# Optimization experiments

Hardware: AMD Instinct MI355X
Metric: run time of the kernel (lower is better)

Reference implementation:

```python
import jax, jax.numpy as jnp
import numpy as np

N_NODES = 50000
N_EDGES = 800000
D_IN = 128
D_OUT = 128
NUM_RELS = 100


def setup_inputs() -> dict:
    key = jax.random.key(0)
    k1, k2, k3, k4, k5, k6, k7 = jax.random.split(key, 7)
    h = jax.random.normal(k1, (N_NODES, D_IN), dtype=jnp.float32)
    W = jax.random.normal(k2, (D_IN, D_OUT), dtype=jnp.float32) * 0.05
    attn = jax.random.normal(k3, (2 * D_OUT,), dtype=jnp.float32) * 0.05
    rel_emb = jax.random.normal(k4, (NUM_RELS, 1), dtype=jnp.float32)
    src = jax.random.randint(k5, (N_EDGES,), 0, N_NODES, dtype=jnp.int32)
    dst = jax.random.randint(k6, (N_EDGES,), 0, N_NODES, dtype=jnp.int32)
    etype = jax.random.randint(k7, (N_EDGES,), 0, NUM_RELS, dtype=jnp.int32)
    return {"h": h, "W": W, "attn": attn, "rel_emb": rel_emb,
            "src": src, "dst": dst, "etype": etype}


def reference(h, W, attn, rel_emb, src, dst, etype):
    # h: [N, d_in], W: [d_in, d_out], attn: [2*d_out], rel_emb: [R, 1]
    # src/dst/etype: [E]
    N = h.shape[0]
    d = W.shape[1]
    # padding_idx=0 in nn.Embedding -> row 0 is zero
    rel_table = rel_emb.at[0].set(0.0)
    z = h @ W  # [N, d_out]
    # attn_fc([z_src, z_dst]) = z_src @ a_l + z_dst @ a_r (split the concat-linear)
    s_src = z @ attn[:d]  # [N]
    s_dst = z @ attn[d:]  # [N]
    e = jax.nn.leaky_relu(s_src[src] + s_dst[dst])  # [E], slope 0.01 as in torch
    # segment softmax over incoming edges of each dst node
    m = jax.ops.segment_max(e, dst, num_segments=N)  # [N]
    ex = jnp.exp(e - m[dst])  # [E]
    denom = jax.ops.segment_sum(ex, dst, num_segments=N)  # [N]
    alpha = ex / denom[dst]  # [E]
    coef = rel_table[etype, 0] * alpha  # [E]  (rel_alpha * alpha)
    # weighted sum of source messages per destination node
    out = jax.ops.segment_sum(coef[:, None] * z[src], dst, num_segments=N)  # [N, d_out]
    return out
```

## Files before the change

kernel.cpp:

```cpp
#include <hip/hip_runtime.h>

#define D 128
#define GROWS 64

typedef __attribute__((ext_vector_type(8))) short short8;
typedef __attribute__((ext_vector_type(4))) float float4v;

__device__ __forceinline__ ushort f2bf(float x) {
    uint u = __float_as_uint(x);
    return (ushort)((u + 0x7FFFu + ((u >> 16) & 1u)) >> 16);
}
__device__ __forceinline__ float bf_lo(uint u) { return __uint_as_float(u << 16); }
__device__ __forceinline__ float bf_hi(uint u) { return __uint_as_float(u & 0xFFFF0000u); }

__global__ __launch_bounds__(256) void convW_kernel(
    const float* __restrict__ W, ushort* __restrict__ Wtg)
{
    int idx = blockIdx.x * 256 + threadIdx.x;
    int k = idx >> 7, n = idx & 127;
    Wtg[n * 128 + k] = f2bf(W[idx]);
}

__global__ __launch_bounds__(512) void gemm_mfma_kernel(
    const float* __restrict__ h, const ushort* __restrict__ Wtg,
    const float* __restrict__ attn, const int* __restrict__ dst,
    ushort* __restrict__ zb, float* __restrict__ s_src, float* __restrict__ s_dst,
    int* __restrict__ histm, int nhi, int N, int E, int nblocks)
{
    __shared__ ushort ht[GROWS * 136];
    __shared__ float psum_s[GROWS][2];
    __shared__ float psum_d[GROWS][2];
    __shared__ int histA[256];
    const int tid = threadIdx.x;
    const int base = blockIdx.x * GROWS;

#pragma unroll
    for (int it = 0; it < 4; ++it) {
        int idx = it * 512 + tid;
        int r = idx >> 5, c4 = (idx & 31) * 4;
        float4 v = make_float4(0.f, 0.f, 0.f, 0.f);
        if (base + r < N) v = *(const float4*)&h[(size_t)(base + r) * D + c4];
        ushort4 u = make_ushort4(f2bf(v.x), f2bf(v.y), f2bf(v.z), f2bf(v.w));
        *(ushort4*)&ht[r * 136 + c4] = u;
    }
    if (tid < 256) histA[tid] = 0;
    __syncthreads();

    const int lane = tid & 63;
    const int wave = tid >> 6;
    const int wr = wave >> 1;
    const int wc = wave & 1;
    const int col = lane & 15;
    const int quad = lane >> 4;
    const int wm = wr * 16;

    float4v acc[4];
#pragma unroll
    for (int nt = 0; nt < 4; ++nt) acc[nt] = (float4v)(0.f);

#pragma unroll 1
    for (int kc = 0; kc < 128; kc += 32) {
        short8 a = *(const short8*)&ht[(wm + col) * 136 + kc + quad * 8];
#pragma unroll
        for (int nt = 0; nt < 4; ++nt) {
            short8 b = *(const short8*)&Wtg[(wc * 64 + nt * 16 + col) * 128 + kc + quad * 8];
            acc[nt] = __builtin_amdgcn_mfma_f32_16x16x32_bf16(a, b, acc[nt], 0, 0, 0);
        }
    }
    __syncthreads();

    float ps[4] = {0.f, 0.f, 0.f, 0.f}, pd[4] = {0.f, 0.f, 0.f, 0.f};
#pragma unroll
    for (int nt = 0; nt < 4; ++nt) {
        float aL = attn[wc * 64 + nt * 16 + col];
        float aR = attn[D + wc * 64 + nt * 16 + col];
#pragma unroll
        for (int reg = 0; reg < 4; ++reg) {
            float v = acc[nt][reg];
            ps[reg] = fmaf(v, aL, ps[reg]);
            pd[reg] = fmaf(v, aR, pd[reg]);
            ht[(wm + quad * 4 + reg) * 136 + wc * 64 + nt * 16 + col] = f2bf(v);
        }
    }
#pragma unroll
    for (int reg = 0; reg < 4; ++reg) {
#pragma unroll
        for (int off = 1; off < 16; off <<= 1) {
            ps[reg] += __shfl_xor(ps[reg], off);
            pd[reg] += __shfl_xor(pd[reg], off);
        }
        if (col == 0) {
            int rl = wm + quad * 4 + reg;
            psum_s[rl][wc] = ps[reg];
            psum_d[rl][wc] = pd[reg];
        }
    }
    __syncthreads();

    if (tid < GROWS && base + tid < N) {
        s_src[base + tid] = psum_s[tid][0] + psum_s[tid][1];
        s_dst[base + tid] = psum_d[tid][0] + psum_d[tid][1];
    }

#pragma unroll
    for (int it = 0; it < 2; ++it) {
        int idx = it * 512 + tid;
        int r = idx >> 4, c8 = idx & 15;
        if (base + r < N)
            *(uint4*)&zb[(size_t)(base + r) * D + c8 * 8] = *(uint4*)&ht[r * 136 + c8 * 8];
    }

    const int cpb = (E + nblocks - 1) / nblocks;
    const int cs = blockIdx.x * cpb;
    const int ce = min(cs + cpb, E);
    for (int i = cs + tid; i < ce; i += 512)
        atomicAdd(&histA[dst[i] >> 8], 1);
    __syncthreads();
    if (tid < nhi) histm[blockIdx.x * nhi + tid] = histA[tid];
}

__global__ __launch_bounds__(64) void binB1_kernel(
    int* __restrict__ histm, int* __restrict__ colsum, int nhi, int nchunk)
{
    const int b = blockIdx.x;
    const int t = threadIdx.x;
    const int K = (nchunk + 63) / 64;
    int v[16];
    int s = 0;
#pragma unroll
    for (int j = 0; j < 16; ++j) {
        int c = t * K + j;
        v[j] = (j < K && c < nchunk) ? histm[c * nhi + b] : 0;
        s += v[j];
    }
    int incl = s;
#pragma unroll
    for (int off = 1; off < 64; off <<= 1) {
        int u = __shfl_up(incl, off);
        if (t >= off) incl += u;
    }
    int run = incl - s;
#pragma unroll
    for (int j = 0; j < 16; ++j) {
        int c = t * K + j;
        if (j < K && c < nchunk) { histm[c * nhi + b] = run; run += v[j]; }
    }
    if (t == 63) colsum[b] = incl;
}

__global__ __launch_bounds__(256) void binC_kernel(
    const int* __restrict__ src, const int* __restrict__ dst,
    const int* __restrict__ etype, const int* __restrict__ histm,
    const int* __restrict__ colsum, uint* __restrict__ binned,
    int nhi, int E, int nchunk)
{
    __shared__ int sc[256];
    __shared__ int cur[256];
    const int tid = threadIdx.x;
    int tot = (tid < nhi) ? colsum[tid] : 0;
    sc[tid] = tot;
    __syncthreads();
    for (int off = 1; off < 256; off <<= 1) {
        int u = (tid >= off) ? sc[tid - off] : 0;
        __syncthreads();
        sc[tid] += u;
        __syncthreads();
    }
    if (tid < nhi) cur[tid] = (sc[tid] - tot) + histm[blockIdx.x * nhi + tid];
    __syncthreads();
    const int cpb = (E + nchunk - 1) / nchunk;
    const int cs = blockIdx.x * cpb;
    const int ce = min(cs + cpb, E);
    for (int i = cs + tid; i < ce; i += 256) {
        int d = dst[i];
        int pos = atomicAdd(&cur[d >> 8], 1);
        binned[pos] = (uint)src[i] | ((uint)etype[i] << 16) | ((uint)(d & 255) << 23);
    }
}

__global__ __launch_bounds__(256) void binD_kernel(
    const uint* __restrict__ binned, const int* __restrict__ colsum,
    int* __restrict__ offsets, uint* __restrict__ csr, int nhi, int N, int E)
{
    __shared__ int sc[256];
    __shared__ int hist[256];
    __shared__ int cur[256];
    const int t = threadIdx.x;
    const int hi = blockIdx.x;
    int tot = (t < nhi) ? colsum[t] : 0;
    sc[t] = tot;
    __syncthreads();
    for (int off = 1; off < 256; off <<= 1) {
        int u = (t >= off) ? sc[t - off] : 0;
        __syncthreads();
        sc[t] += u;
        __syncthreads();
    }
    const int bb = (hi == 0) ? 0 : sc[hi - 1];
    const int be = sc[hi];
    hist[t] = 0;
    __syncthreads();
    for (int i = bb + t; i < be; i += 256)
        atomicAdd(&hist[(binned[i] >> 23) & 0xFF], 1);
    __syncthreads();
    int total = hist[t];
    cur[t] = total;
    __syncthreads();
    for (int off = 1; off < 256; off <<= 1) {
        int u = (t >= off) ? cur[t - off] : 0;
        __syncthreads();
        cur[t] += u;
        __syncthreads();
    }
    int excl = cur[t] - total;
    int node = hi * 256 + t;
    if (node < N) offsets[node] = bb + excl;
    if (node == N - 1) offsets[N] = E;
    __syncthreads();
    cur[t] = bb + excl;
    __syncthreads();
    for (int i = bb + t; i < be; i += 256) {
        uint pk = binned[i];
        int pos = atomicAdd(&cur[(pk >> 23) & 0xFF], 1);
        csr[pos] = pk;
    }
}

__global__ __launch_bounds__(256) void aggregate_kernel(
    const uint* __restrict__ zb32, const float* __restrict__ s_src,
    const float* __restrict__ s_dst, const int* __restrict__ offsets,
    const uint* __restrict__ csr_packed, const float* __restrict__ rel_emb,
    float* __restrict__ out, int N, int R)
{
    __shared__ float rel_l[128];
    const int tid = threadIdx.x;
    if (tid < R) rel_l[tid] = (tid == 0) ? 0.f : rel_emb[tid];
    __syncthreads();

    const int lane = tid & 63;
    const int half = lane & 31;
    const int hsel = lane >> 5;
    const int d = blockIdx.x * 4 + (tid >> 6);
    if (d >= N) return;

    const int start = offsets[d];
    const int end = offsets[d + 1];
    const float sdst = s_dst[d];

    float m = -INFINITY, l = 0.f;
    float4 acc = make_float4(0.f, 0.f, 0.f, 0.f);

    for (int base = start; base < end; base += 64) {
        const int idx = base + lane;
        const bool valid = idx < end;
        const uint packed = valid ? csr_packed[idx] : 0;
        const int srcv = (int)(packed & 0xFFFF);
        const int et = (int)((packed >> 16) & 0x7F);
        float ev = -INFINITY;
        if (valid) {
            float x = s_src[srcv] + sdst;
            ev = (x > 0.f) ? x : 0.01f * x;
        }
        float cm = ev;
#pragma unroll
        for (int off = 32; off; off >>= 1) cm = fmaxf(cm, __shfl_xor(cm, off));
        const float newm = fmaxf(m, cm);
        const float scale = __expf(m - newm);
        const float p = valid ? __expf(ev - newm) : 0.f;
        float ssum = p;
#pragma unroll
        for (int off = 32; off; off >>= 1) ssum += __shfl_xor(ssum, off);
        l = l * scale + ssum;
        acc.x *= scale; acc.y *= scale; acc.z *= scale; acc.w *= scale;
        m = newm;

        const float w = p * rel_l[et];
        const int nv = min(64, end - base);
        for (int j = 0; j < nv; j += 8) {
            const int e0 = j + hsel, e1 = j + 2 + hsel, e2 = j + 4 + hsel, e3 = j + 6 + hsel;
            const float w0 = __shfl(w, e0), w1 = __shfl(w, e1);
            const float w2 = __shfl(w, e2), w3 = __shfl(w, e3);
            const int s0 = __shfl(srcv, e0), s1 = __shfl(srcv, e1);
            const int s2 = __shfl(srcv, e2), s3 = __shfl(srcv, e3);
            const uint2 u0 = *(const uint2*)(zb32 + (size_t)s0 * 64 + half * 2);
            const uint2 u1 = *(const uint2*)(zb32 + (size_t)s1 * 64 + half * 2);
            const uint2 u2 = *(const uint2*)(zb32 + (size_t)s2 * 64 + half * 2);
            const uint2 u3 = *(const uint2*)(zb32 + (size_t)s3 * 64 + half * 2);
            acc.x = fmaf(w0, bf_lo(u0.x), acc.x);
            acc.y = fmaf(w0, bf_hi(u0.x), acc.y);
            acc.z = fmaf(w0, bf_lo(u0.y), acc.z);
            acc.w = fmaf(w0, bf_hi(u0.y), acc.w);
            acc.x = fmaf(w1, bf_lo(u1.x), acc.x);
            acc.y = fmaf(w1, bf_hi(u1.x), acc.y);
            acc.z = fmaf(w1, bf_lo(u1.y), acc.z);
            acc.w = fmaf(w1, bf_hi(u1.y), acc.w);
            acc.x = fmaf(w2, bf_lo(u2.x), acc.x);
            acc.y = fmaf(w2, bf_hi(u2.x), acc.y);
            acc.z = fmaf(w2, bf_lo(u2.y), acc.z);
            acc.w = fmaf(w2, bf_hi(u2.y), acc.w);
            acc.x = fmaf(w3, bf_lo(u3.x), acc.x);
            acc.y = fmaf(w3, bf_hi(u3.x), acc.y);
            acc.z = fmaf(w3, bf_lo(u3.y), acc.z);
            acc.w = fmaf(w3, bf_hi(u3.y), acc.w);
        }
    }

    acc.x += __shfl_xor(acc.x, 32);
    acc.y += __shfl_xor(acc.y, 32);
    acc.z += __shfl_xor(acc.z, 32);
    acc.w += __shfl_xor(acc.w, 32);

    const float inv = (l > 0.f) ? 1.0f / l : 0.f;
    if (lane < 32) {
        float4 res = make_float4(acc.x * inv, acc.y * inv, acc.z * inv, acc.w * inv);
        *(float4*)(out + (size_t)d * D + 4 * half) = res;
    }
}

extern "C" void kernel_launch(void* const* d_in, const int* in_sizes, int n_in,
                              void* d_out, int out_size, void* d_ws, size_t ws_size,
                              hipStream_t stream)
{
    const float* h    = (const float*)d_in[0];
    const float* W    = (const float*)d_in[1];
    const float* attn = (const float*)d_in[2];
    const float* rel  = (const float*)d_in[3];
    const int*   src  = (const int*)d_in[4];
    const int*   dst  = (const int*)d_in[5];
    const int*   et   = (const int*)d_in[6];
    float* out = (float*)d_out;

    const int N = in_sizes[0] / D;
    const int E = in_sizes[4];
    const int R = in_sizes[3];

    char* p = (char*)d_ws;
    auto alloc = [&](size_t bytes) {
        char* q = p;
        p += (bytes + 255) & ~(size_t)255;
        return q;
    };
    const int nhi     = (N + 255) / 256;
    const int gblocks = (N + GROWS - 1) / GROWS;

    ushort* zb     = (ushort*)alloc((size_t)N * D * sizeof(ushort));
    ushort* Wtg    = (ushort*)alloc((size_t)D * D * sizeof(ushort));
    float* ssrc    = (float*)alloc((size_t)N * sizeof(float));
    float* sdst    = (float*)alloc((size_t)N * sizeof(float));
    int*   offsets = (int*)alloc((size_t)(N + 1) * sizeof(int));
    uint*  binned  = (uint*)alloc((size_t)E * sizeof(uint));
    uint*  csr     = (uint*)alloc((size_t)E * sizeof(uint));
    int*   histm   = (int*)alloc((size_t)gblocks * nhi * sizeof(int));
    int*   colsum  = (int*)alloc((size_t)nhi * sizeof(int));

    convW_kernel<<<64, 256, 0, stream>>>(W, Wtg);
    gemm_mfma_kernel<<<gblocks, 512, 0, stream>>>(h, Wtg, attn, dst, zb, ssrc, sdst,
                                                  histm, nhi, N, E, gblocks);
    binB1_kernel<<<nhi, 64, 0, stream>>>(histm, colsum, nhi, gblocks);
    binC_kernel<<<gblocks, 256, 0, stream>>>(src, dst, et, histm, colsum, binned,
                                             nhi, E, gblocks);
    binD_kernel<<<nhi, 256, 0, stream>>>(binned, colsum, offsets, csr, nhi, N, E);
    aggregate_kernel<<<(N + 3) / 4, 256, 0, stream>>>((const uint*)zb, ssrc, sdst,
                                                      offsets, csr, rel, out, N, R);
}
```

Measured before the change: 172.2 us.

## Assign quarter-wave per destination node in aggregation and unroll GEMM k-loop

The aggregation kernel now gives each 16-lane quarter of a wave one destination node, so a wave handles 4 nodes. Each lane loads 16 bytes of the bf16 source row, where it previously loaded 8. With about 16 edges per node on average, the old 64-lane chunking left most lanes idle, and this mapping is meant to cut that waste and the cross-half reduction. Shuffle reductions now cover 16 lanes and the grid is 4x smaller. The GEMM k-loop is also fully unrolled. Nodes with widely different degrees inside one wave may now cause divergence.

Measured after the change: 165.7 us. 1.04x faster.

```diff
diff --git a/kernel.cpp b/kernel.cpp
--- a/kernel.cpp
+++ b/kernel.cpp
@@ -58,7 +58,7 @@
 #pragma unroll
     for (int nt = 0; nt < 4; ++nt) acc[nt] = (float4v)(0.f);
 
-#pragma unroll 1
+#pragma unroll
     for (int kc = 0; kc < 128; kc += 32) {
         short8 a = *(const short8*)&ht[(wm + col) * 136 + kc + quad * 8];
 #pragma unroll
@@ -238,20 +238,23 @@
     __syncthreads();
 
     const int lane = tid & 63;
-    const int half = lane & 31;
-    const int hsel = lane >> 5;
-    const int d = blockIdx.x * 4 + (tid >> 6);
+    const int q    = lane >> 4;
+    const int ql   = lane & 15;
+    const int wave = tid >> 6;
+    const int d = blockIdx.x * 16 + wave * 4 + q;
     if (d >= N) return;
 
     const int start = offsets[d];
-    const int end = offsets[d + 1];
+    const int end   = offsets[d + 1];
     const float sdst = s_dst[d];
+    const int qb = q * 16;
 
     float m = -INFINITY, l = 0.f;
-    float4 acc = make_float4(0.f, 0.f, 0.f, 0.f);
-
-    for (int base = start; base < end; base += 64) {
-        const int idx = base + lane;
+    float4 acc0 = make_float4(0.f, 0.f, 0.f, 0.f);
+    float4 acc1 = make_float4(0.f, 0.f, 0.f, 0.f);
+
+    for (int base = start; base < end; base += 16) {
+        const int idx = base + ql;
         const bool valid = idx < end;
         const uint packed = valid ? csr_packed[idx] : 0;
         const int srcv = (int)(packed & 0xFFFF);
@@ -263,58 +266,72 @@
         }
         float cm = ev;
 #pragma unroll
-        for (int off = 32; off; off >>= 1) cm = fmaxf(cm, __shfl_xor(cm, off));
+        for (int off = 8; off; off >>= 1) cm = fmaxf(cm, __shfl_xor(cm, off));
         const float newm = fmaxf(m, cm);
         const float scale = __expf(m - newm);
         const float p = valid ? __expf(ev - newm) : 0.f;
         float ssum = p;
 #pragma unroll
-        for (int off = 32; off; off >>= 1) ssum += __shfl_xor(ssum, off);
+        for (int off = 8; off; off >>= 1) ssum += __shfl_xor(ssum, off);
         l = l * scale + ssum;
-        acc.x *= scale; acc.y *= scale; acc.z *= scale; acc.w *= scale;
+        acc0.x *= scale; acc0.y *= scale; acc0.z *= scale; acc0.w *= scale;
+        acc1.x *= scale; acc1.y *= scale; acc1.z *= scale; acc1.w *= scale;
         m = newm;
 
         const float w = p * rel_l[et];
-        const int nv = min(64, end - base);
-        for (int j = 0; j < nv; j += 8) {
-            const int e0 = j + hsel, e1 = j + 2 + hsel, e2 = j + 4 + hsel, e3 = j + 6 + hsel;
-            const float w0 = __shfl(w, e0), w1 = __shfl(w, e1);
-            const float w2 = __shfl(w, e2), w3 = __shfl(w, e3);
-            const int s0 = __shfl(srcv, e0), s1 = __shfl(srcv, e1);
-            const int s2 = __shfl(srcv, e2), s3 = __shfl(srcv, e3);
-            const uint2 u0 = *(const uint2*)(zb32 + (size_t)s0 * 64 + half * 2);
-            const uint2 u1 = *(const uint2*)(zb32 + (size_t)s1 * 64 + half * 2);
-            const uint2 u2 = *(const uint2*)(zb32 + (size_t)s2 * 64 + half * 2);
-            const uint2 u3 = *(const uint2*)(zb32 + (size_t)s3 * 64 + half * 2);
-            acc.x = fmaf(w0, bf_lo(u0.x), acc.x);
-            acc.y = fmaf(w0, bf_hi(u0.x), acc.y);
-            acc.z = fmaf(w0, bf_lo(u0.y), acc.z);
-            acc.w = fmaf(w0, bf_hi(u0.y), acc.w);
-            acc.x = fmaf(w1, bf_lo(u1.x), acc.x);
-            acc.y = fmaf(w1, bf_hi(u1.x), acc.y);
-            acc.z = fmaf(w1, bf_lo(u1.y), acc.z);
-            acc.w = fmaf(w1, bf_hi(u1.y), acc.w);
-            acc.x = fmaf(w2, bf_lo(u2.x), acc.x);
-            acc.y = fmaf(w2, bf_hi(u2.x), acc.y);
-            acc.z = fmaf(w2, bf_lo(u2.y), acc.z);
-            acc.w = fmaf(w2, bf_hi(u2.y), acc.w);
-            acc.x = fmaf(w3, bf_lo(u3.x), acc.x);
-            acc.y = fmaf(w3, bf_hi(u3.x), acc.y);
-            acc.z = fmaf(w3, bf_lo(u3.y), acc.z);
-            acc.w = fmaf(w3, bf_hi(u3.y), acc.w);
-        }
-    }
-
-    acc.x += __shfl_xor(acc.x, 32);
-    acc.y += __shfl_xor(acc.y, 32);
-    acc.z += __shfl_xor(acc.z, 32);
-    acc.w += __shfl_xor(acc.w, 32);
+        const int nv = min(16, end - base);
+        for (int j = 0; j < nv; j += 4) {
+            const float w0 = __shfl(w, qb + j);
+            const float w1 = __shfl(w, qb + j + 1);
+            const float w2 = __shfl(w, qb + j + 2);
+            const float w3 = __shfl(w, qb + j + 3);
+            const int s0 = __shfl(srcv, qb + j);
+            const int s1 = __shfl(srcv, qb + j + 1);
+            const int s2 = __shfl(srcv, qb + j + 2);
+            const int s3 = __shfl(srcv, qb + j + 3);
+            const uint4 u0 = *(const uint4*)(zb32 + (size_t)s0 * 64 + ql * 4);
+            const uint4 u1 = *(const uint4*)(zb32 + (size_t)s1 * 64 + ql * 4);
+            const uint4 u2 = *(const uint4*)(zb32 + (size_t)s2 * 64 + ql * 4);
+            const uint4 u3 = *(const uint4*)(zb32 + (size_t)s3 * 64 + ql * 4);
+            acc0.x = fmaf(w0, bf_lo(u0.x), acc0.x);
+            acc0.y = fmaf(w0, bf_hi(u0.x), acc0.y);
+            acc0.z = fmaf(w0, bf_lo(u0.y), acc0.z);
+            acc0.w = fmaf(w0, bf_hi(u0.y), acc0.w);
+            acc1.x = fmaf(w0, bf_lo(u0.z), acc1.x);
+            acc1.y = fmaf(w0, bf_hi(u0.z), acc1.y);
+            acc1.z = fmaf(w0, bf_lo(u0.w), acc1.z);
+            acc1.w = fmaf(w0, bf_hi(u0.w), acc1.w);
+            acc0.x = fmaf(w1, bf_lo(u1.x), acc0.x);
+            acc0.y = fmaf(w1, bf_hi(u1.x), acc0.y);
+            acc0.z = fmaf(w1, bf_lo(u1.y), acc0.z);
+            acc0.w = fmaf(w1, bf_hi(u1.y), acc0.w);
+            acc1.x = fmaf(w1, bf_lo(u1.z), acc1.x);
+            acc1.y = fmaf(w1, bf_hi(u1.z), acc1.y);
+            acc1.z = fmaf(w1, bf_lo(u1.w), acc1.z);
+            acc1.w = fmaf(w1, bf_hi(u1.w), acc1.w);
+            acc0.x = fmaf(w2, bf_lo(u2.x), acc0.x);
+            acc0.y = fmaf(w2, bf_hi(u2.x), acc0.y);
+            acc0.z = fmaf(w2, bf_lo(u2.y), acc0.z);
+            acc0.w = fmaf(w2, bf_hi(u2.y), acc0.w);
+            acc1.x = fmaf(w2, bf_lo(u2.z), acc1.x);
+            acc1.y = fmaf(w2, bf_hi(u2.z), acc1.y);
+            acc1.z = fmaf(w2, bf_lo(u2.w), acc1.z);
+            acc1.w = fmaf(w2, bf_hi(u2.w), acc1.w);
+            acc0.x = fmaf(w3, bf_lo(u3.x), acc0.x);
+            acc0.y = fmaf(w3, bf_hi(u3.x), acc0.y);
+            acc0.z = fmaf(w3, bf_lo(u3.y), acc0.z);
+            acc0.w = fmaf(w3, bf_hi(u3.y), acc0.w);
+            acc1.x = fmaf(w3, bf_lo(u3.z), acc1.x);
+            acc1.y = fmaf(w3, bf_hi(u3.z), acc1.y);
+            acc1.z = fmaf(w3, bf_lo(u3.w), acc1.z);
+            acc1.w = fmaf(w3, bf_hi(u3.w), acc1.w);
+        }
+    }
 
     const float inv = (l > 0.f) ? 1.0f / l : 0.f;
-    if (lane < 32) {
-        float4 res = make_float4(acc.x * inv, acc.y * inv, acc.z * inv, acc.w * inv);
-        *(float4*)(out + (size_t)d * D + 4 * half) = res;
-    }
+    float* orow = out + (size_t)d * D + ql * 8;
+    *(float4*)orow       = make_float4(acc0.x * inv, acc0.y * inv, acc0.z * inv, acc0.w * inv);
+    *(float4*)(orow + 4) = make_float4(acc1.x * inv, acc1.y * inv, acc1.z * inv, acc1.w * inv);
 }
 
 extern "C" void kernel_launch(void* const* d_in, const int* in_sizes, int n_in,
@@ -360,6 +377,6 @@
     binC_kernel<<<gblocks, 256, 0, stream>>>(src, dst, et, histm, colsum, binned,
                                              nhi, E, gblocks);
     binD_kernel<<<nhi, 256, 0, stream>>>(binned, colsum, offsets, csr, nhi, N, E);
-    aggregate_kernel<<<(N + 3) / 4, 256, 0, stream>>>((const uint*)zb, ssrc, sdst,
-                                                      offsets, csr, rel, out, N, R);
-}
+    aggregate_kernel<<<(N + 15) / 16, 256, 0, stream>>>((const uint*)zb, ssrc, sdst,
+                                                        offsets, csr, rel, out, N, R);
+}
```
